# Performance work log

Measured on AMD Instinct MI355X. Metric: run time of the kernel, lower is better.

Reference implementation:

```python
import jax, jax.numpy as jnp
import numpy as np
import math

# ---- Clifford algebra Cl(3,0,1) (PGA) tables, blade dim = 2^4 = 16 ----

def _popcount(x):
    return bin(x).count("1")

def _swap_sign(a, b):
    # sign of reordering basis vectors when multiplying blade a by blade b
    a >>= 1
    s = 0
    while a:
        s += _popcount(a & b)
        a >>= 1
    return -1.0 if (s & 1) else 1.0

def _tables():
    # blades ordered by grade (then bitmask): matches subspaces [1,4,6,4,1]
    blades = sorted(range(16), key=lambda m: (_popcount(m), m))
    idx = {m: i for i, m in enumerate(blades)}
    grade = np.array([_popcount(m) for m in blades])
    gp = np.zeros((16, 16, 16), np.float32)  # geometric product: e_j e_k = sum_i gp[i,j,k] e_i
    jp = np.zeros((16, 16, 16), np.float32)  # join (dual of wedge of duals)
    s_comp = {m: _swap_sign(m, 15 ^ m) for m in range(16)}  # e_m ^ e_{~m} = s_comp[m] * e_{1111}
    for j, mj in enumerate(blades):
        for k, mk in enumerate(blades):
            common = mj & mk
            # metric: e0^2 = 0 (bit 0), e1..e3 square to +1 -> zero iff e0 repeated
            if not (common & 1):
                gp[idx[mj ^ mk], j, k] = _swap_sign(mj, mk)
            cj, ck = 15 ^ mj, 15 ^ mk
            if not (cj & ck):  # duals wedge to nonzero
                r = mj & mk  # join blade = intersection
                jp[idx[r], j, k] = s_comp[mj] * s_comp[mk] * _swap_sign(cj, ck) * s_comp[r]
    return gp, jp, grade

GP_T, JP_T, GRADE = _tables()
SUBSPACES = np.array([math.comb(4, i) for i in range(5)])  # [1,4,6,4,1]

def _paths(mt):
    p = np.zeros((5, 5, 5), bool)
    for i in range(5):
        for j in range(5):
            for k in range(5):
                p[i, j, k] = np.any(mt[np.ix_(GRADE == i, GRADE == j, GRADE == k)] != 0)
    return p

GP_PATHS = _paths(GP_T)
JP_PATHS = _paths(JP_T)
GP_IDX = np.nonzero(GP_PATHS)  # static index triples for scatter
JP_IDX = np.nonzero(JP_PATHS)


def _expand(w_sparse, path_idx):
    # [C, n_paths] -> scatter into [C,5,5,5] -> repeat_interleave by subspaces -> [C,16,16,16]
    C = w_sparse.shape[0]
    w5 = jnp.zeros((C, 5, 5, 5), w_sparse.dtype).at[:, path_idx[0], path_idx[1], path_idx[2]].set(w_sparse)
    g = jnp.asarray(GRADE)
    return w5[:, g][:, :, g][:, :, :, g]


def setup_inputs() -> dict:
    key = jax.random.key(0)
    k1, k2, k3, k4 = jax.random.split(key, 4)
    C = 64
    B = 65536  # flattened batch*residues tokens
    std = 1.0 / math.sqrt(5.0)
    x = jax.random.normal(k1, (B, C, 16), dtype=jnp.float32)
    gp_weights = std * jax.random.normal(k2, (C, int(GP_PATHS.sum())), dtype=jnp.float32)
    jp_weights = std * jax.random.normal(k3, (C, int(JP_PATHS.sum())), dtype=jnp.float32)
    # MVLinear(C -> 2C): one weight per (out, in, grade), no bias
    lin_weight = jax.random.normal(k4, (2 * C, C, 5), dtype=jnp.float32) / math.sqrt(C)
    return {"x": x, "gp_weights": gp_weights, "jp_weights": jp_weights, "lin_weight": lin_weight}


def reference(x, gp_weights, jp_weights, lin_weight):
    C = gp_weights.shape[0]
    # rebuild dense [C,16,16,16] bilinear weight from sparse grade-path coefficients
    W = jnp.asarray(GP_T)[None] * _expand(gp_weights, GP_IDX) \
      + jnp.asarray(JP_T)[None] * _expand(jp_weights, JP_IDX)
    # grade-equivariant linear C -> 2C (weight shared within each grade)
    Wb = lin_weight[:, :, jnp.asarray(GRADE)]          # [2C, C, 16]
    y = jnp.einsum('oib,...ib->...ob', Wb, x)          # [..., 2C, 16]
    y1, y2 = y[..., :C, :], y[..., C:, :]
    # trilinear geometric+join product, with residual on second half
    return jnp.einsum('nijk,...nj,...nk->...ni', W, y1, y2) + y2
```

## Files before the change

### kernel.cpp

```cpp
#include <hip/hip_runtime.h>

#define NQ 273

typedef float f4 __attribute__((ext_vector_type(4)));

struct GATab {
  int qi[NQ]; int qj[NQ]; int qk[NQ];
  float qs[NQ];
  int qgp[NQ];
  int qpath[NQ];
  int qnew[NQ];
  int ngp, njp, nq;
};

constexpr int popc4(int m){ int c=0; for(int b=0;b<5;++b) c+=(m>>b)&1; return c; }
constexpr int swap_par(int a,int b){ int s=0; a>>=1; while(a){ s+=popc4(a&b); a>>=1; } return s&1; }

constexpr GATab make_tab(){
  GATab t{};
  int bladeOf[16]={}; int idxOf[16]={};
  { int p=0;
    for(int g=0; g<=4; ++g)
      for(int m=0; m<16; ++m)
        if(popc4(m)==g){ bladeOf[p]=m; idxOf[m]=p; ++p; }
  }
  int grade[16]={};
  for(int j=0;j<16;++j) grade[j]=popc4(bladeOf[j]);
  bool gpp[125]={}; bool jpp[125]={};
  for(int j=0;j<16;++j) for(int k=0;k<16;++k){
    int mj=bladeOf[j], mk=bladeOf[k];
    if(!(mj&mk&1)){ int i=idxOf[mj^mk]; gpp[(grade[i]*5+grade[j])*5+grade[k]]=true; }
    int cj=15^mj, ck=15^mk;
    if(!(cj&ck)){ int r=mj&mk; int i=idxOf[r]; jpp[(grade[i]*5+grade[j])*5+grade[k]]=true; }
  }
  int gpidx[125]={}; int jpidx[125]={};
  { int c=0; for(int u=0;u<125;++u){ gpidx[u] = gpp[u]? c++ : -1; } t.ngp=c; }
  { int c=0; for(int u=0;u<125;++u){ jpidx[u] = jpp[u]? c++ : -1; } t.njp=c; }
  int q=0;
  for(int j=0;j<16;++j) for(int k=0;k<16;++k){
    int mj=bladeOf[j], mk=bladeOf[k];
    if(!(mj&mk&1)){
      int i=idxOf[mj^mk];
      t.qi[q]=i; t.qj[q]=j; t.qk[q]=k;
      t.qs[q] = swap_par(mj,mk) ? -1.0f : 1.0f;
      t.qgp[q]=1;
      t.qpath[q]=gpidx[(grade[i]*5+grade[j])*5+grade[k]];
      ++q;
    }
  }
  for(int j=0;j<16;++j) for(int k=0;k<16;++k){
    int mj=bladeOf[j], mk=bladeOf[k];
    int cj=15^mj, ck=15^mk;
    if(!(cj&ck)){
      int r=mj&mk; int i=idxOf[r];
      int par = swap_par(mj,15^mj) ^ swap_par(mk,15^mk) ^ swap_par(cj,ck) ^ swap_par(r,15^r);
      t.qi[q]=i; t.qj[q]=j; t.qk[q]=k;
      t.qs[q] = par ? -1.0f : 1.0f;
      t.qgp[q]=0;
      t.qpath[q]=jpidx[(grade[i]*5+grade[j])*5+grade[k]];
      ++q;
    }
  }
  t.nq=q;

  for(int a=1;a<t.nq;++a){
    int ci=t.qi[a], cj2=t.qj[a], ck2=t.qk[a], cg=t.qgp[a], cp=t.qpath[a]; float cs=t.qs[a];
    int key = cg ? cp : 1000+cp;
    int b=a-1;
    while(b>=0){
      int kb = t.qgp[b] ? t.qpath[b] : 1000+t.qpath[b];
      if(kb <= key) break;
      t.qi[b+1]=t.qi[b]; t.qj[b+1]=t.qj[b]; t.qk[b+1]=t.qk[b];
      t.qs[b+1]=t.qs[b]; t.qgp[b+1]=t.qgp[b]; t.qpath[b+1]=t.qpath[b];
      --b;
    }
    t.qi[b+1]=ci; t.qj[b+1]=cj2; t.qk[b+1]=ck2; t.qs[b+1]=cs; t.qgp[b+1]=cg; t.qpath[b+1]=cp;
  }
  for(int a=0;a<t.nq;++a){
    if(a==0){ t.qnew[a]=1; continue; }
    int ka = t.qgp[a]   ? t.qpath[a]   : 1000+t.qpath[a];
    int kb = t.qgp[a-1] ? t.qpath[a-1] : 1000+t.qpath[a-1];
    t.qnew[a] = (ka!=kb) ? 1 : 0;
  }
  return t;
}

constexpr GATab TAB = make_tab();
static_assert(TAB.nq == NQ, "nonzero count mismatch");
static_assert(TAB.ngp > 0 && TAB.njp > 0, "path counts");
constexpr int NGPC = TAB.ngp;
constexpr int NJPC = TAB.njp;
constexpr int GR[16] = {0,1,1,1,1,2,2,2,2,2,2,3,3,3,3,4};

constexpr int PADG = (NGPC & 1) ? NGPC : NGPC + 1;
constexpr int PADJ = (NJPC & 1) ? NJPC : NJPC + 1;
constexpr int CGF  = 64 * PADG;
constexpr int CJF  = 64 * PADJ;
constexpr int XLF  = 4 * 64 * 16;
static_assert((CGF + CJF + XLF) * 4 <= 32 * 1024, "5 blocks/CU requires <=32KB");

__global__ void prep_wrp(const float* __restrict__ linw, float* __restrict__ wrp){
  int t = blockIdx.x*blockDim.x + threadIdx.x;
  if(t < 64*64*12){
    int s = t % 12;
    int n = (t/12) & 63;
    int i = t/(12*64);
    float v = 0.f;
    if(s < 5)       v = linw[(n*64 + i)*5 + s];
    else if(s < 10) v = linw[((64+n)*64 + i)*5 + (s-5)];
    wrp[t] = v;
  }
}

__global__ void prep_cpk(const float* __restrict__ gpw, const float* __restrict__ jpw,
                         float* __restrict__ cgj){
  int n = threadIdx.x;
  for(int p=0;p<NGPC;++p) cgj[n*PADG + p] = gpw[n*NGPC + p];
  for(int p=0;p<NJPC;++p) cgj[CGF + n*PADJ + p] = jpw[n*NJPC + p];
}

__global__ __launch_bounds__(256)
void main_k(const float* __restrict__ x, const float* __restrict__ cgj,
            const float* __restrict__ wrp, float* __restrict__ out, int B){
  __shared__ float lds[CGF + CJF + XLF];
  float* clg = lds;
  float* clj = lds + CGF;
  float* xl  = lds + CGF + CJF;

  const int tid  = threadIdx.x;
  const int lane = tid & 63;
  const int wv   = tid >> 6;
  const int n    = lane;

  for(int idx = tid; idx < CGF + CJF; idx += 256) lds[idx] = cgj[idx];
  __syncthreads();

  const int cgbase = n*PADG;
  const int cjbase = n*PADJ;
  float* xw = xl + wv*1024;

  for(int base = blockIdx.x*4; base < B; base += gridDim.x*4){
    const int bb = base + wv;

    if(bb < B){
      const f4* src = (const f4*)(x + ((long)bb*64 + lane)*16);
      #pragma unroll
      for(int r=0;r<4;++r){
        f4 a = __builtin_nontemporal_load(src+r);
        int daddr = (lane*16 + r*4) ^ ((lane&7)<<2);
        *(f4*)(xw + daddr) = a;
      }
    }

    float y1[16], y2[16];
    #pragma unroll
    for(int v=0;v<16;++v){ y1[v]=0.f; y2[v]=0.f; }

    #pragma unroll 2
    for(int i=0;i<64;++i){
      const f4* wp = (const f4*)(wrp + (i*64 + n)*12);
      f4 wa = wp[0], wb = wp[1], wc = wp[2];
      float w1[5] = {wa[0],wa[1],wa[2],wa[3],wb[0]};
      float w2[5] = {wb[1],wb[2],wb[3],wc[0],wc[1]};

      float xv[16];
      #pragma unroll
      for(int g=0;g<4;++g){
        int raddr = (i*16 + g*4) ^ ((i&7)<<2);
        f4 a = *(const f4*)(xw + raddr);
        xv[g*4+0]=a[0]; xv[g*4+1]=a[1]; xv[g*4+2]=a[2]; xv[g*4+3]=a[3];
      }

      #pragma unroll
      for(int v=0;v<16;++v){
        y1[v] = fmaf(w1[GR[v]], xv[v], y1[v]);
        y2[v] = fmaf(w2[GR[v]], xv[v], y2[v]);
      }
    }

    __builtin_amdgcn_sched_barrier(0x7);
    float acc[16];
    #pragma unroll
    for(int v=0;v<16;++v) acc[v]=y2[v];

    float c = 0.f;
    #pragma unroll
    for(int q=0;q<NQ;++q){
      if(TAB.qnew[q])
        c = TAB.qgp[q] ? clg[cgbase + TAB.qpath[q]] : clj[cjbase + TAB.qpath[q]];
      float prod = y1[TAB.qj[q]] * y2[TAB.qk[q]];
      acc[TAB.qi[q]] = fmaf((TAB.qs[q] < 0.f) ? -c : c, prod, acc[TAB.qi[q]]);
      if((q % 24) == 23) __builtin_amdgcn_sched_barrier(0x7);
    }
    __builtin_amdgcn_sched_barrier(0x7);

    if(bb < B){
      f4* op = (f4*)(out + ((long)bb*64 + n)*16);
      #pragma unroll
      for(int r=0;r<4;++r){
        f4 o; o[0]=acc[4*r]; o[1]=acc[4*r+1]; o[2]=acc[4*r+2]; o[3]=acc[4*r+3];
        __builtin_nontemporal_store(o, op+r);
      }
    }
  }
}

extern "C" void kernel_launch(void* const* d_in, const int* in_sizes, int n_in,
                              void* d_out, int out_size, void* d_ws, size_t ws_size,
                              hipStream_t stream){
  const float* x    = (const float*)d_in[0];
  const float* gpw  = (const float*)d_in[1];
  const float* jpw  = (const float*)d_in[2];
  const float* linw = (const float*)d_in[3];
  float* outp = (float*)d_out;

  float* wrp = (float*)d_ws;
  float* cgj = wrp + 64*64*12;

  int B = in_sizes[0] / (64*16);

  prep_wrp <<<192, 256, 0, stream>>>(linw, wrp);
  prep_cpk <<<1,   64,  0, stream>>>(gpw, jpw, cgj);
  main_k   <<<2048, 256, 0, stream>>>(x, cgj, wrp, outp, B);
}
```

Baseline: 552.6 us.

## Pack linear-layer weights and inputs pairwise for packed FP32 FMA

Result: slower. 580.7 us (+5.1%).

```diff
diff --git a/kernel.cpp b/kernel.cpp
--- a/kernel.cpp
+++ b/kernel.cpp
@@ -3,6 +3,7 @@
 #define NQ 273
 
 typedef float f4 __attribute__((ext_vector_type(4)));
+typedef float f2 __attribute__((ext_vector_type(2)));
 
 struct GATab {
   int qi[NQ]; int qj[NQ]; int qk[NQ];
@@ -96,8 +97,8 @@
 constexpr int PADJ = (NJPC & 1) ? NJPC : NJPC + 1;
 constexpr int CGF  = 64 * PADG;
 constexpr int CJF  = 64 * PADJ;
-constexpr int XLF  = 4 * 64 * 16;
-static_assert((CGF + CJF + XLF) * 4 <= 32 * 1024, "5 blocks/CU requires <=32KB");
+constexpr int XLF  = 4 * 64 * 32;
+static_assert((CGF + CJF + XLF) * 4 <= 53 * 1024, "3 blocks/CU requires <=53.3KB");
 
 __global__ void prep_wrp(const float* __restrict__ linw, float* __restrict__ wrp){
   int t = blockIdx.x*blockDim.x + threadIdx.x;
@@ -106,8 +107,10 @@
     int n = (t/12) & 63;
     int i = t/(12*64);
     float v = 0.f;
-    if(s < 5)       v = linw[(n*64 + i)*5 + s];
-    else if(s < 10) v = linw[((64+n)*64 + i)*5 + (s-5)];
+    if(s < 10){
+      int g = s >> 1;
+      v = (s & 1) ? linw[((64+n)*64 + i)*5 + g] : linw[(n*64 + i)*5 + g];
+    }
     wrp[t] = v;
   }
 }
@@ -137,7 +140,7 @@
 
   const int cgbase = n*PADG;
   const int cjbase = n*PADJ;
-  float* xw = xl + wv*1024;
+  float* xw = xl + wv*2048;
 
   for(int base = blockIdx.x*4; base < B; base += gridDim.x*4){
     const int bb = base + wv;
@@ -147,48 +150,51 @@
       #pragma unroll
       for(int r=0;r<4;++r){
         f4 a = __builtin_nontemporal_load(src+r);
-        int daddr = (lane*16 + r*4) ^ ((lane&7)<<2);
-        *(f4*)(xw + daddr) = a;
+        f4 d0 = __builtin_shufflevector(a, a, 0,0,1,1);
+        f4 d1 = __builtin_shufflevector(a, a, 2,2,3,3);
+        int base0 = lane*32 + r*8;
+        *(f4*)(xw + ((base0    ) ^ ((lane&7)<<2))) = d0;
+        *(f4*)(xw + ((base0 + 4) ^ ((lane&7)<<2))) = d1;
       }
     }
 
-    float y1[16], y2[16];
+    f2 y12[16];
     #pragma unroll
-    for(int v=0;v<16;++v){ y1[v]=0.f; y2[v]=0.f; }
+    for(int v=0;v<16;++v) y12[v] = (f2)(0.f);
 
     #pragma unroll 2
     for(int i=0;i<64;++i){
       const f4* wp = (const f4*)(wrp + (i*64 + n)*12);
       f4 wa = wp[0], wb = wp[1], wc = wp[2];
-      float w1[5] = {wa[0],wa[1],wa[2],wa[3],wb[0]};
-      float w2[5] = {wb[1],wb[2],wb[3],wc[0],wc[1]};
-
-      float xv[16];
+      f2 w12[5];
+      w12[0] = __builtin_shufflevector(wa, wa, 0,1);
+      w12[1] = __builtin_shufflevector(wa, wa, 2,3);
+      w12[2] = __builtin_shufflevector(wb, wb, 0,1);
+      w12[3] = __builtin_shufflevector(wb, wb, 2,3);
+      w12[4] = __builtin_shufflevector(wc, wc, 0,1);
+
       #pragma unroll
-      for(int g=0;g<4;++g){
-        int raddr = (i*16 + g*4) ^ ((i&7)<<2);
+      for(int g=0;g<8;++g){
+        int raddr = (i*32 + g*4) ^ ((i&7)<<2);
         f4 a = *(const f4*)(xw + raddr);
-        xv[g*4+0]=a[0]; xv[g*4+1]=a[1]; xv[g*4+2]=a[2]; xv[g*4+3]=a[3];
-      }
-
-      #pragma unroll
-      for(int v=0;v<16;++v){
-        y1[v] = fmaf(w1[GR[v]], xv[v], y1[v]);
-        y2[v] = fmaf(w2[GR[v]], xv[v], y2[v]);
+        f2 p0 = __builtin_shufflevector(a, a, 0,1);
+        f2 p1 = __builtin_shufflevector(a, a, 2,3);
+        y12[2*g]   = __builtin_elementwise_fma(w12[GR[2*g]],   p0, y12[2*g]);
+        y12[2*g+1] = __builtin_elementwise_fma(w12[GR[2*g+1]], p1, y12[2*g+1]);
       }
     }
 
     __builtin_amdgcn_sched_barrier(0x7);
     float acc[16];
     #pragma unroll
-    for(int v=0;v<16;++v) acc[v]=y2[v];
+    for(int v=0;v<16;++v) acc[v] = y12[v][1];
 
     float c = 0.f;
     #pragma unroll
     for(int q=0;q<NQ;++q){
       if(TAB.qnew[q])
         c = TAB.qgp[q] ? clg[cgbase + TAB.qpath[q]] : clj[cjbase + TAB.qpath[q]];
-      float prod = y1[TAB.qj[q]] * y2[TAB.qk[q]];
+      float prod = y12[TAB.qj[q]][0] * y12[TAB.qk[q]][1];
       acc[TAB.qi[q]] = fmaf((TAB.qs[q] < 0.f) ? -c : c, prod, acc[TAB.qi[q]]);
       if((q % 24) == 23) __builtin_amdgcn_sched_barrier(0x7);
     }
@@ -221,5 +227,5 @@
 
   prep_wrp <<<192, 256, 0, stream>>>(linw, wrp);
   prep_cpk <<<1,   64,  0, stream>>>(gpw, jpw, cgj);
-  main_k   <<<2048, 256, 0, stream>>>(x, cgj, wrp, outp, B);
-}
+  main_k   <<<768, 256, 0, stream>>>(x, cgj, wrp, outp, B);
+}
```
